# Performance work log

Hardware: AMD Instinct MI355X
Metric: run time of the kernel (lower is better)

## Reference

```python
import jax, jax.numpy as jnp
import numpy as np

S = 1024      # sequence length
V = 32000     # vocab size
H = 1024      # hidden_dim
A = 128       # attn_size (module default)


def lstm_cell(x, h, c, Wih, Whh, b):
    # torch LSTM gate order: i, f, g, o
    g = x @ Wih.T + h @ Whh.T + b
    i, f, gg, o = jnp.split(g, 4)
    c = jax.nn.sigmoid(f) * c + jax.nn.sigmoid(i) * jnp.tanh(gg)
    h = jax.nn.sigmoid(o) * jnp.tanh(c)
    return h, c


def setup_inputs() -> dict:
    key = jax.random.key(0)
    ks = jax.random.split(key, 16)
    p = lambda k, shape: (jax.random.normal(k, shape, jnp.float32) * 0.02)
    return {
        'input_seq': jax.random.randint(ks[0], (S,), 0, V),
        'gold_seq': jax.random.randint(ks[1], (S,), 0, V),
        'embed': p(ks[2], (V, H)),
        'enc_Wih': p(ks[3], (4 * H, H)),
        'enc_Whh': p(ks[4], (4 * H, H)),
        'enc_b': jnp.zeros((4 * H,), jnp.float32),   # b_ih + b_hh combined
        'dec_Wih': p(ks[5], (4 * H, 2 * H)),          # decoder input = [prev, context]
        'dec_Whh': p(ks[6], (4 * H, H)),
        'dec_b': jnp.zeros((4 * H,), jnp.float32),
        'U_w': p(ks[7], (A, H)), 'U_b': jnp.zeros((A,), jnp.float32),
        'Wa_w': p(ks[8], (A, H)), 'Wa_b': jnp.zeros((A,), jnp.float32),
        'Va_w': p(ks[9], (1, A)), 'Va_b': jnp.zeros((1,), jnp.float32),
        'out_w': p(ks[10], (V, H)), 'out_b': jnp.zeros((V,), jnp.float32),
    }


def reference(input_seq, gold_seq, embed, enc_Wih, enc_Whh, enc_b,
              dec_Wih, dec_Whh, dec_b, U_w, U_b, Wa_w, Wa_b, Va_w, Va_b,
              out_w, out_b):
    Hd = embed.shape[1]
    x_emb = embed[input_seq]  # (S, H)

    def enc_step(carry, x):
        h, c = carry
        h, c = lstm_cell(x, h, c, enc_Wih, enc_Whh, enc_b)
        return (h, c), h

    zero = jnp.zeros((Hd,), x_emb.dtype)
    (h0, c0), enc_out = jax.lax.scan(enc_step, (zero, zero), x_emb)  # enc_out: (S, H)

    U_enc = enc_out @ U_w.T + U_b  # (S, A), hidden-independent part of additive attention

    # teacher forcing: prev_0 = zeros, prev_i = embed(gold[i-1]); relu applied each step
    prev = jnp.concatenate([jnp.zeros((1, Hd), x_emb.dtype), embed[gold_seq[:-1]]], axis=0)
    prev = jax.nn.relu(prev)  # (S, H)

    def dec_step(carry, p):
        h, c = carry
        # additive attention scores: V(tanh(U(enc) + W(h)))  -> (S, 1)
        scores = jnp.tanh(U_enc + h @ Wa_w.T + Wa_b) @ Va_w.T + Va_b
        # faithful to nn.Softmax() on a (S,1) tensor: torch picks dim=1 -> all ones
        w = jax.nn.softmax(scores, axis=1)  # (S, 1), == ones
        context = w[:, 0] @ enc_out         # (H,) == sum of encoder outputs
        x = jnp.concatenate([p, context])   # (2H,)
        h, c = lstm_cell(x, h, c, dec_Wih, dec_Whh, dec_b)
        logits = h @ out_w.T + out_b        # (V,)
        return (h, c), (logits, jnp.argmax(logits))

    _, (preds, idxs) = jax.lax.scan(dec_step, (h0, c0), prev)
    return preds, idxs  # (S, V) float logits, (S,) predicted ids
```

## Files before the change

### kernel.cpp

```cpp
#include <hip/hip_runtime.h>
#include <math.h>


#define S_LEN 1024
#define HDIM  1024
#define VDIM  32000

typedef float f4 __attribute__((ext_vector_type(4)));

__device__ __forceinline__ void agent_storef(float* p, float v) {
    __hip_atomic_store(p, v, __ATOMIC_RELAXED, __HIP_MEMORY_SCOPE_AGENT);
}
__device__ __forceinline__ float sigmoidf_(float x) {
    return 1.0f / (1.0f + expf(-x));
}
__device__ __forceinline__ void llc_load_4x4(const float* p, f4& a, f4& b,
                                             f4& c, f4& d) {
    asm volatile(
        "global_load_dwordx4 %0, %4, off sc0 sc1\n\t"
        "global_load_dwordx4 %1, %4, off offset:1024 sc0 sc1\n\t"
        "global_load_dwordx4 %2, %4, off offset:2048 sc0 sc1\n\t"
        "global_load_dwordx4 %3, %4, off offset:3072 sc0 sc1\n\t"
        "s_waitcnt vmcnt(0)"
        : "=&v"(a), "=&v"(b), "=&v"(c), "=&v"(d)
        : "v"(p) : "memory");
}
__device__ __forceinline__ int swz(int s) {
    return (s & ~7) | ((s ^ (s >> 3)) & 7);
}

template<int MODE>
__global__ __launch_bounds__(256)
void gemm_nt(const float* __restrict__ A, int lda,
             const float* __restrict__ B, int ldb,
             const float* __restrict__ bias,
             float* __restrict__ C, int ldc,
             const float* __restrict__ embed,
             const int* __restrict__ gidx,
             int M, int N, int K)
{
    __shared__ float As[16][128];
    __shared__ float Bs[16][128];

    const int tid = threadIdx.x;
    const int m0 = blockIdx.y * 128;
    const int n0 = blockIdx.x * 128;

    float acc[8][8];
#pragma unroll
    for (int r = 0; r < 8; ++r)
#pragma unroll
        for (int c = 0; c < 8; ++c) acc[r][c] = 0.0f;

    const int ty = tid >> 4;
    const int tx = tid & 15;

    for (int k0 = 0; k0 < K; k0 += 16) {
#pragma unroll
        for (int q = 0; q < 2; ++q) {
            int id = tid * 2 + q;
            int m  = id >> 2;
            int c4 = (id & 3) * 4;
            float4 v;
            if (MODE == 0) {
                v = *(const float4*)(A + (size_t)(m0 + m) * lda + k0 + c4);
            } else if (MODE == 1) {
                int row = gidx[m0 + m];
                v = *(const float4*)(embed + (size_t)row * HDIM + k0 + c4);
            } else {
                int mg = m0 + m;
                if (mg == 0) {
                    v = make_float4(0.f, 0.f, 0.f, 0.f);
                } else {
                    int row = gidx[mg - 1];
                    v = *(const float4*)(embed + (size_t)row * HDIM + k0 + c4);
                    v.x = fmaxf(v.x, 0.f); v.y = fmaxf(v.y, 0.f);
                    v.z = fmaxf(v.z, 0.f); v.w = fmaxf(v.w, 0.f);
                }
            }
            As[c4 + 0][m] = v.x; As[c4 + 1][m] = v.y;
            As[c4 + 2][m] = v.z; As[c4 + 3][m] = v.w;
        }
#pragma unroll
        for (int q = 0; q < 2; ++q) {
            int id = tid * 2 + q;
            int n  = id >> 2;
            int c4 = (id & 3) * 4;
            float4 v = *(const float4*)(B + (size_t)(n0 + n) * ldb + k0 + c4);
            Bs[c4 + 0][n] = v.x; Bs[c4 + 1][n] = v.y;
            Bs[c4 + 2][n] = v.z; Bs[c4 + 3][n] = v.w;
        }
        __syncthreads();

#pragma unroll
        for (int k = 0; k < 16; ++k) {
            float4 a0 = *(const float4*)&As[k][ty * 8];
            float4 a1 = *(const float4*)&As[k][ty * 8 + 4];
            float4 b0 = *(const float4*)&Bs[k][tx * 8];
            float4 b1 = *(const float4*)&Bs[k][tx * 8 + 4];
            float av[8] = {a0.x,a0.y,a0.z,a0.w,a1.x,a1.y,a1.z,a1.w};
            float bv[8] = {b0.x,b0.y,b0.z,b0.w,b1.x,b1.y,b1.z,b1.w};
#pragma unroll
            for (int r = 0; r < 8; ++r)
#pragma unroll
                for (int c = 0; c < 8; ++c)
                    acc[r][c] = fmaf(av[r], bv[c], acc[r][c]);
        }
        __syncthreads();
    }

    const int mbase = m0 + ty * 8;
    const int nbase = n0 + tx * 8;
#pragma unroll
    for (int r = 0; r < 8; ++r) {
        float4 o0, o1;
        o0.x = acc[r][0] + bias[nbase + 0];
        o0.y = acc[r][1] + bias[nbase + 1];
        o0.z = acc[r][2] + bias[nbase + 2];
        o0.w = acc[r][3] + bias[nbase + 3];
        o1.x = acc[r][4] + bias[nbase + 4];
        o1.y = acc[r][5] + bias[nbase + 5];
        o1.z = acc[r][6] + bias[nbase + 6];
        o1.w = acc[r][7] + bias[nbase + 7];
        *(float4*)(C + (size_t)(mbase + r) * ldc + nbase)     = o0;
        *(float4*)(C + (size_t)(mbase + r) * ldc + nbase + 4) = o1;
    }
}

__global__ __launch_bounds__(512, 2)
void lstm_seq(const float* __restrict__ Whh,
              const float* __restrict__ G,
              const float* __restrict__ h_init,
              const float* __restrict__ c_init,
              float* __restrict__ h_out,
              float* __restrict__ c_fin,
              float* __restrict__ csum_out,
              int slen)
{
    __shared__ f4 hbuf[256];
    const int tid = threadIdx.x;
    const int g   = blockIdx.x;
    const int wv  = tid >> 6;
    const int lg  = tid & 63;
    const int j   = g * 8 + wv;

    f4 W[4][4];
#pragma unroll
    for (int q = 0; q < 4; ++q)
#pragma unroll
        for (int i = 0; i < 4; ++i)
            W[q][i] = *(const f4*)(Whh + (size_t)(j + q * HDIM) * HDIM
                                   + 4 * lg + 256 * i);

    float c = 0.0f, csum = 0.0f;
    if (lg == 0) c = c_init[j];

    float gnow = G[(size_t)(lg & 3) * HDIM + j];

    for (int t = 0; t < slen; ++t) {
#pragma unroll
        for (int q = 0; q < 4; ++q)
#pragma unroll
            for (int i = 0; i < 4; ++i)
                asm volatile("" : "+v"(W[q][i]));

        const float* hp = (t == 0) ? h_init : (h_out + (size_t)(t - 1) * HDIM);

        if (wv == 0) {
            f4 a, b, cc, d;
            const float* p = hp + 4 * lg;
            for (;;) {
                llc_load_4x4(p, a, b, cc, d);
                float s0 = (a.x + a.y) + (a.z + a.w);
                float s1 = (b.x + b.y) + (b.z + b.w);
                float s2 = (cc.x + cc.y) + (cc.z + cc.w);
                float s3 = (d.x + d.y) + (d.z + d.w);
                float s  = (s0 + s1) + (s2 + s3);
                if (!__any(s != s)) break;
                __builtin_amdgcn_s_sleep(1);
            }
            hbuf[swz(lg)]       = a;
            hbuf[swz(64 + lg)]  = b;
            hbuf[swz(128 + lg)] = cc;
            hbuf[swz(192 + lg)] = d;
        }
        __syncthreads();

        int tn = (t + 1 < slen) ? (t + 1) : t;
        float gnext = G[(size_t)tn * (4 * HDIM) + (lg & 3) * HDIM + j];

        f4 h0 = hbuf[swz(lg)];
        f4 h1 = hbuf[swz(64 + lg)];
        f4 h2 = hbuf[swz(128 + lg)];
        f4 h3 = hbuf[swz(192 + lg)];
        float p0 = 0.f, p1 = 0.f, p2 = 0.f, p3 = 0.f;
        f4 hv;
#pragma unroll
        for (int i = 0; i < 4; ++i) {
            hv = (i == 0) ? h0 : (i == 1) ? h1 : (i == 2) ? h2 : h3;
            p0 = fmaf(W[0][i].x, hv.x, fmaf(W[0][i].y, hv.y,
                 fmaf(W[0][i].z, hv.z, fmaf(W[0][i].w, hv.w, p0))));
            p1 = fmaf(W[1][i].x, hv.x, fmaf(W[1][i].y, hv.y,
                 fmaf(W[1][i].z, hv.z, fmaf(W[1][i].w, hv.w, p1))));
            p2 = fmaf(W[2][i].x, hv.x, fmaf(W[2][i].y, hv.y,
                 fmaf(W[2][i].z, hv.z, fmaf(W[2][i].w, hv.w, p2))));
            p3 = fmaf(W[3][i].x, hv.x, fmaf(W[3][i].y, hv.y,
                 fmaf(W[3][i].z, hv.z, fmaf(W[3][i].w, hv.w, p3))));
        }

        float t01 = __shfl_xor((lg & 1) ? p0 : p1, 1);
        float s01 = ((lg & 1) ? p1 : p0) + t01;
        float t23 = __shfl_xor((lg & 1) ? p2 : p3, 1);
        float s23 = ((lg & 1) ? p3 : p2) + t23;
        float tq  = __shfl_xor((lg & 2) ? s01 : s23, 2);
        float s   = ((lg & 2) ? s23 : s01) + tq;
        s += __shfl_xor(s, 4);
        s += __shfl_xor(s, 8);
        s += __shfl_xor(s, 16);
        s += __shfl_xor(s, 32);

        float pre = s + gnow;
        float act = ((lg & 3) == 2) ? tanhf(pre) : sigmoidf_(pre);
        float a1 = __shfl(act, 1);
        float a2 = __shfl(act, 2);
        float a3 = __shfl(act, 3);

        if (lg == 0) {
            c = a1 * c + act * a2;
            float h = a3 * tanhf(c);
            csum += h;
            agent_storef(h_out + (size_t)t * HDIM + j, h);
        }
        gnow = gnext;

        __syncthreads();
    }

    if (lg == 0) {
        if (c_fin)    c_fin[j]    = c;
        if (csum_out) csum_out[j] = csum;
    }
}

__global__ __launch_bounds__(256)
void ctx_bias_k(const float* __restrict__ dec_Wih,
                const float* __restrict__ dec_b,
                const float* __restrict__ ctx,
                float* __restrict__ out)
{
    const int wv = threadIdx.x >> 6;
    const int lane = threadIdx.x & 63;
    const int r = blockIdx.x * 4 + wv;
    const float* wr = dec_Wih + (size_t)r * (2 * HDIM) + HDIM;
    float s = 0.f;
    for (int k = lane; k < HDIM; k += 64) s += wr[k] * ctx[k];
#pragma unroll
    for (int off = 32; off > 0; off >>= 1) s += __shfl_xor(s, off);
    if (lane == 0) out[r] = s + dec_b[r];
}

__global__ __launch_bounds__(256)
void argmax_k(const float* __restrict__ logits, float* __restrict__ out_idx)
{
    __shared__ float bv[256];
    __shared__ int   bidx[256];
    const int row = blockIdx.x;
    const int tid = threadIdx.x;
    const float* p = logits + (size_t)row * VDIM;
    float best = -INFINITY;
    int   bi   = 0;
    for (int v = tid; v < VDIM; v += 256) {
        float x = p[v];
        if (x > best) { best = x; bi = v; }
    }
    bv[tid] = best; bidx[tid] = bi;
    __syncthreads();
    for (int s = 128; s > 0; s >>= 1) {
        if (tid < s) {
            if (bv[tid + s] > bv[tid] ||
                (bv[tid + s] == bv[tid] && bidx[tid + s] < bidx[tid])) {
                bv[tid] = bv[tid + s];
                bidx[tid] = bidx[tid + s];
            }
        }
        __syncthreads();
    }
    if (tid == 0) out_idx[row] = (float)bidx[0];
}

extern "C" void kernel_launch(void* const* d_in, const int* in_sizes, int n_in,
                              void* d_out, int out_size, void* d_ws, size_t ws_size,
                              hipStream_t stream)
{
    (void)in_sizes; (void)n_in; (void)out_size; (void)ws_size;

    const int*   input_seq = (const int*)d_in[0];
    const int*   gold_seq  = (const int*)d_in[1];
    const float* embed     = (const float*)d_in[2];
    const float* enc_Wih   = (const float*)d_in[3];
    const float* enc_Whh   = (const float*)d_in[4];
    const float* enc_b     = (const float*)d_in[5];
    const float* dec_Wih   = (const float*)d_in[6];
    const float* dec_Whh   = (const float*)d_in[7];
    const float* dec_b     = (const float*)d_in[8];
    const float* out_w     = (const float*)d_in[15];
    const float* out_b     = (const float*)d_in[16];

    float* out = (float*)d_out;

    float* G_enc = out;
    float* G_dec = out + 4194304;

    float* zerovec   = (float*)d_ws + 256;
    float* c0        = zerovec + 1024;
    float* ctx       = c0 + 1024;
    float* ctxb      = ctx + 1024;
    float* enc_out   = ctxb + 4096;
    float* dec_h     = enc_out + 1048576;

    hipMemsetAsync(d_ws, 0, 5120, stream);
    hipMemsetAsync(enc_out, 0xFF, (size_t)S_LEN * HDIM * 4, stream);
    hipMemsetAsync(dec_h,   0xFF, (size_t)S_LEN * HDIM * 4, stream);

    dim3 blk(256);

    gemm_nt<1><<<dim3(32, 8), blk, 0, stream>>>(
        nullptr, 0, enc_Wih, HDIM, enc_b, G_enc, 4 * HDIM,
        embed, input_seq, S_LEN, 4 * HDIM, HDIM);

    lstm_seq<<<128, dim3(512), 0, stream>>>(
        enc_Whh, G_enc, zerovec, zerovec, enc_out, c0, ctx, S_LEN);

    ctx_bias_k<<<1024, blk, 0, stream>>>(dec_Wih, dec_b, ctx, ctxb);

    gemm_nt<2><<<dim3(32, 8), blk, 0, stream>>>(
        nullptr, 0, dec_Wih, 2 * HDIM, ctxb, G_dec, 4 * HDIM,
        embed, gold_seq, S_LEN, 4 * HDIM, HDIM);

    lstm_seq<<<128, dim3(512), 0, stream>>>(
        dec_Whh, G_dec, enc_out + (size_t)(S_LEN - 1) * HDIM, c0,
        dec_h, nullptr, nullptr, S_LEN);

    gemm_nt<0><<<dim3(VDIM / 128, 8), blk, 0, stream>>>(
        dec_h, HDIM, out_w, HDIM, out_b, out, VDIM,
        nullptr, nullptr, S_LEN, VDIM, HDIM);

    argmax_k<<<1024, blk, 0, stream>>>(out, out + (size_t)S_LEN * VDIM);
}
```

Baseline: 5.335 ms.

## Use split-bf16 MFMA for logits GEMM with fused argmax and merged input GEMMs

Replaces the fp32 SIMT logits GEMM with a bf16 MFMA kernel that splits each fp32 operand into hi/lo bf16 parts and runs three MFMAs to keep near-fp32 accuracy. Argmax is fused into the GEMM epilogue through a packed 64-bit atomicMax key, which removes the separate pass that re-read the full logits matrix. The encoder and decoder input-projection GEMMs are merged into one launch, with the context bias added inside the decoder LSTM instead of inside the GEMM. The risks are numerical differences from the bf16 split possibly changing argmax ties, plus atomic contention.

```diff
diff --git a/kernel.cpp b/kernel.cpp
--- a/kernel.cpp
+++ b/kernel.cpp
@@ -7,6 +7,8 @@
 #define VDIM  32000
 
 typedef float f4 __attribute__((ext_vector_type(4)));
+typedef float f32x4 __attribute__((ext_vector_type(4)));
+typedef short short8 __attribute__((ext_vector_type(8)));
 
 __device__ __forceinline__ void agent_storef(float* p, float v) {
     __hip_atomic_store(p, v, __ATOMIC_RELAXED, __HIP_MEMORY_SCOPE_AGENT);
@@ -25,26 +27,39 @@
         : "=&v"(a), "=&v"(b), "=&v"(c), "=&v"(d)
         : "v"(p) : "memory");
 }
+__device__ __forceinline__ bool any_nan16(f4 a, f4 b, f4 c, f4 d) {
+    float s0 = (a.x + a.y) + (a.z + a.w);
+    float s1 = (b.x + b.y) + (b.z + b.w);
+    float s2 = (c.x + c.y) + (c.z + c.w);
+    float s3 = (d.x + d.y) + (d.z + d.w);
+    float s  = (s0 + s1) + (s2 + s3);
+    return s != s;
+}
 __device__ __forceinline__ int swz(int s) {
     return (s & ~7) | ((s ^ (s >> 3)) & 7);
 }
+__device__ __forceinline__ void split_bf16(float x, unsigned short& h,
+                                           unsigned short& l) {
+    unsigned u = __float_as_uint(x);
+    unsigned hr = (u + 0x7FFFu + ((u >> 16) & 1u)) >> 16;
+    h = (unsigned short)hr;
+    float hf = __uint_as_float(hr << 16);
+    float r = x - hf;
+    unsigned v = __float_as_uint(r);
+    l = (unsigned short)((v + 0x7FFFu + ((v >> 16) & 1u)) >> 16);
+}
 
 template<int MODE>
-__global__ __launch_bounds__(256)
-void gemm_nt(const float* __restrict__ A, int lda,
-             const float* __restrict__ B, int ldb,
-             const float* __restrict__ bias,
-             float* __restrict__ C, int ldc,
-             const float* __restrict__ embed,
-             const int* __restrict__ gidx,
-             int M, int N, int K)
+__device__ void gemm_body(const float* __restrict__ B, int ldb,
+                          const float* __restrict__ bias,
+                          float* __restrict__ C, int ldc,
+                          const float* __restrict__ embed,
+                          const int* __restrict__ gidx,
+                          int m0, int n0, int K)
 {
     __shared__ float As[16][128];
     __shared__ float Bs[16][128];
-
     const int tid = threadIdx.x;
-    const int m0 = blockIdx.y * 128;
-    const int n0 = blockIdx.x * 128;
 
     float acc[8][8];
 #pragma unroll
@@ -62,9 +77,7 @@
             int m  = id >> 2;
             int c4 = (id & 3) * 4;
             float4 v;
-            if (MODE == 0) {
-                v = *(const float4*)(A + (size_t)(m0 + m) * lda + k0 + c4);
-            } else if (MODE == 1) {
+            if (MODE == 1) {
                 int row = gidx[m0 + m];
                 v = *(const float4*)(embed + (size_t)row * HDIM + k0 + c4);
             } else {
@@ -91,7 +104,6 @@
             Bs[c4 + 2][n] = v.z; Bs[c4 + 3][n] = v.w;
         }
         __syncthreads();
-
 #pragma unroll
         for (int k = 0; k < 16; ++k) {
             float4 a0 = *(const float4*)&As[k][ty * 8];
@@ -114,28 +126,52 @@
 #pragma unroll
     for (int r = 0; r < 8; ++r) {
         float4 o0, o1;
-        o0.x = acc[r][0] + bias[nbase + 0];
-        o0.y = acc[r][1] + bias[nbase + 1];
-        o0.z = acc[r][2] + bias[nbase + 2];
-        o0.w = acc[r][3] + bias[nbase + 3];
-        o1.x = acc[r][4] + bias[nbase + 4];
-        o1.y = acc[r][5] + bias[nbase + 5];
-        o1.z = acc[r][6] + bias[nbase + 6];
-        o1.w = acc[r][7] + bias[nbase + 7];
+        float b0 = (MODE == 2) ? 0.f : bias[nbase + 0];
+        float b1 = (MODE == 2) ? 0.f : bias[nbase + 1];
+        float b2 = (MODE == 2) ? 0.f : bias[nbase + 2];
+        float b3 = (MODE == 2) ? 0.f : bias[nbase + 3];
+        float b4 = (MODE == 2) ? 0.f : bias[nbase + 4];
+        float b5 = (MODE == 2) ? 0.f : bias[nbase + 5];
+        float b6 = (MODE == 2) ? 0.f : bias[nbase + 6];
+        float b7 = (MODE == 2) ? 0.f : bias[nbase + 7];
+        o0.x = acc[r][0] + b0; o0.y = acc[r][1] + b1;
+        o0.z = acc[r][2] + b2; o0.w = acc[r][3] + b3;
+        o1.x = acc[r][4] + b4; o1.y = acc[r][5] + b5;
+        o1.z = acc[r][6] + b6; o1.w = acc[r][7] + b7;
         *(float4*)(C + (size_t)(mbase + r) * ldc + nbase)     = o0;
         *(float4*)(C + (size_t)(mbase + r) * ldc + nbase + 4) = o1;
     }
 }
 
-__global__ __launch_bounds__(512, 2)
-void lstm_seq(const float* __restrict__ Whh,
-              const float* __restrict__ G,
-              const float* __restrict__ h_init,
-              const float* __restrict__ c_init,
-              float* __restrict__ h_out,
-              float* __restrict__ c_fin,
-              float* __restrict__ csum_out,
-              int slen)
+__global__ __launch_bounds__(256)
+void g_both(const float* __restrict__ embed,
+            const int* __restrict__ input_seq,
+            const int* __restrict__ gold_seq,
+            const float* __restrict__ enc_Wih,
+            const float* __restrict__ enc_b,
+            const float* __restrict__ dec_Wih,
+            float* __restrict__ G_enc,
+            float* __restrict__ G_dec)
+{
+    const int bx = blockIdx.x, by = blockIdx.y;
+    if (by < 8)
+        gemm_body<1>(enc_Wih, HDIM, enc_b, G_enc, 4 * HDIM,
+                     embed, input_seq, by * 128, bx * 128, HDIM);
+    else
+        gemm_body<2>(dec_Wih, 2 * HDIM, nullptr, G_dec, 4 * HDIM,
+                     embed, gold_seq, (by - 8) * 128, bx * 128, HDIM);
+}
+
+template<int GCTX>
+__device__ void lstm_body(const float* __restrict__ Whh,
+                          const float* __restrict__ G,
+                          const float* __restrict__ gctx_vec,
+                          const float* __restrict__ h_init,
+                          const float* __restrict__ c_init,
+                          float* __restrict__ h_out,
+                          float* __restrict__ c_fin,
+                          float* __restrict__ csum_out,
+                          int slen)
 {
     __shared__ f4 hbuf[256];
     const int tid = threadIdx.x;
@@ -155,7 +191,10 @@
     float c = 0.0f, csum = 0.0f;
     if (lg == 0) c = c_init[j];
 
-    float gnow = G[(size_t)(lg & 3) * HDIM + j];
+    float gctx = 0.0f;
+    if (GCTX) gctx = gctx_vec[(size_t)(lg & 3) * HDIM + j];
+
+    float gnow = G[(size_t)(lg & 3) * HDIM + j] + gctx;
 
     for (int t = 0; t < slen; ++t) {
 #pragma unroll
@@ -171,12 +210,7 @@
             const float* p = hp + 4 * lg;
             for (;;) {
                 llc_load_4x4(p, a, b, cc, d);
-                float s0 = (a.x + a.y) + (a.z + a.w);
-                float s1 = (b.x + b.y) + (b.z + b.w);
-                float s2 = (cc.x + cc.y) + (cc.z + cc.w);
-                float s3 = (d.x + d.y) + (d.z + d.w);
-                float s  = (s0 + s1) + (s2 + s3);
-                if (!__any(s != s)) break;
+                if (!__any(any_nan16(a, b, cc, d))) break;
                 __builtin_amdgcn_s_sleep(1);
             }
             hbuf[swz(lg)]       = a;
@@ -187,7 +221,7 @@
         __syncthreads();
 
         int tn = (t + 1 < slen) ? (t + 1) : t;
-        float gnext = G[(size_t)tn * (4 * HDIM) + (lg & 3) * HDIM + j];
+        float gnext = G[(size_t)tn * (4 * HDIM) + (lg & 3) * HDIM + j] + gctx;
 
         f4 h0 = hbuf[swz(lg)];
         f4 h1 = hbuf[swz(64 + lg)];
@@ -232,7 +266,6 @@
             agent_storef(h_out + (size_t)t * HDIM + j, h);
         }
         gnow = gnext;
-
         __syncthreads();
     }
 
@@ -240,6 +273,24 @@
         if (c_fin)    c_fin[j]    = c;
         if (csum_out) csum_out[j] = csum;
     }
+}
+
+__global__ __launch_bounds__(512, 2)
+void lstm_seq(const float* __restrict__ Whh, const float* __restrict__ G,
+              const float* __restrict__ h_init, const float* __restrict__ c_init,
+              float* __restrict__ h_out, float* __restrict__ c_fin,
+              float* __restrict__ csum_out, int slen)
+{
+    lstm_body<0>(Whh, G, nullptr, h_init, c_init, h_out, c_fin, csum_out, slen);
+}
+
+__global__ __launch_bounds__(512, 2)
+void dec_lstm(const float* __restrict__ Whh, const float* __restrict__ G,
+              const float* __restrict__ ctxb, const float* __restrict__ h_init,
+              const float* __restrict__ c_init, float* __restrict__ h_out,
+              int slen)
+{
+    lstm_body<1>(Whh, G, ctxb, h_init, c_init, h_out, nullptr, nullptr, slen);
 }
 
 __global__ __launch_bounds__(256)
@@ -259,33 +310,121 @@
     if (lane == 0) out[r] = s + dec_b[r];
 }
 
+#define LSTR 40
+
+__global__ __launch_bounds__(256, 1)
+void logits_mfma(const float* __restrict__ Amat,
+                 const float* __restrict__ Bmat,
+                 const float* __restrict__ bias,
+                 float* __restrict__ C,
+                 unsigned long long* __restrict__ amax)
+{
+    __shared__ unsigned short Ah[128][LSTR], Al[128][LSTR];
+    __shared__ unsigned short Bh[128][LSTR], Bl[128][LSTR];
+
+    const int tid = threadIdx.x;
+    const int l   = tid & 63;
+    const int w   = tid >> 6;
+    const int n0  = blockIdx.x * 128;
+    const int m0  = blockIdx.y * 128;
+    const int mb  = (w >> 1) * 64;
+    const int nb  = (w & 1) * 64;
+
+    f32x4 acc[4][4];
+#pragma unroll
+    for (int i = 0; i < 4; ++i)
+#pragma unroll
+        for (int j = 0; j < 4; ++j) acc[i][j] = (f32x4){0.f, 0.f, 0.f, 0.f};
+
+    for (int k0 = 0; k0 < HDIM; k0 += 32) {
+#pragma unroll
+        for (int q = 0; q < 4; ++q) {
+            int id  = q * 256 + tid;
+            int row = id >> 3;
+            int kq  = (id & 7) * 4;
+            float4 av = *(const float4*)(Amat + (size_t)(m0 + row) * HDIM
+                                         + k0 + kq);
+            float4 bv = *(const float4*)(Bmat + (size_t)(n0 + row) * HDIM
+                                         + k0 + kq);
+            unsigned short h0,h1,h2,h3, l0,l1,l2,l3;
+            split_bf16(av.x, h0, l0); split_bf16(av.y, h1, l1);
+            split_bf16(av.z, h2, l2); split_bf16(av.w, h3, l3);
+            Ah[row][kq+0]=h0; Ah[row][kq+1]=h1; Ah[row][kq+2]=h2; Ah[row][kq+3]=h3;
+            Al[row][kq+0]=l0; Al[row][kq+1]=l1; Al[row][kq+2]=l2; Al[row][kq+3]=l3;
+            split_bf16(bv.x, h0, l0); split_bf16(bv.y, h1, l1);
+            split_bf16(bv.z, h2, l2); split_bf16(bv.w, h3, l3);
+            Bh[row][kq+0]=h0; Bh[row][kq+1]=h1; Bh[row][kq+2]=h2; Bh[row][kq+3]=h3;
+            Bl[row][kq+0]=l0; Bl[row][kq+1]=l1; Bl[row][kq+2]=l2; Bl[row][kq+3]=l3;
+        }
+        __syncthreads();
+
+        const int kb = (l >> 4) * 8;
+        short8 a_hi[4], a_lo[4], b_hi[4], b_lo[4];
+#pragma unroll
+        for (int i = 0; i < 4; ++i) {
+            int ra = mb + i * 16 + (l & 15);
+            int rb = nb + i * 16 + (l & 15);
+            a_hi[i] = *(const short8*)&Ah[ra][kb];
+            a_lo[i] = *(const short8*)&Al[ra][kb];
+            b_hi[i] = *(const short8*)&Bh[rb][kb];
+            b_lo[i] = *(const short8*)&Bl[rb][kb];
+        }
+#pragma unroll
+        for (int i = 0; i < 4; ++i)
+#pragma unroll
+            for (int j = 0; j < 4; ++j) {
+                acc[i][j] = __builtin_amdgcn_mfma_f32_16x16x32_bf16(
+                    a_hi[i], b_hi[j], acc[i][j], 0, 0, 0);
+                acc[i][j] = __builtin_amdgcn_mfma_f32_16x16x32_bf16(
+                    a_hi[i], b_lo[j], acc[i][j], 0, 0, 0);
+                acc[i][j] = __builtin_amdgcn_mfma_f32_16x16x32_bf16(
+                    a_lo[i], b_hi[j], acc[i][j], 0, 0, 0);
+            }
+        __syncthreads();
+    }
+
+#pragma unroll
+    for (int i = 0; i < 4; ++i) {
+        const int mrow = m0 + mb + i * 16 + ((l >> 4) << 2);
+        unsigned long long key[4] = {0ull, 0ull, 0ull, 0ull};
+#pragma unroll
+        for (int j = 0; j < 4; ++j) {
+            int n = n0 + nb + j * 16 + (l & 15);
+            float bv = bias[n];
+            f32x4 o = acc[i][j];
+#pragma unroll
+            for (int r = 0; r < 4; ++r) {
+                float val = o[r] + bv;
+                C[(size_t)(mrow + r) * VDIM + n] = val;
+                unsigned um = __float_as_uint(val);
+                um = (um & 0x80000000u) ? ~um : (um | 0x80000000u);
+                unsigned long long k2 = ((unsigned long long)um << 32)
+                    | (unsigned long long)(0xFFFFFFFFu - (unsigned)n);
+                if (k2 > key[r]) key[r] = k2;
+            }
+        }
+#pragma unroll
+        for (int r = 0; r < 4; ++r) {
+#pragma unroll
+            for (int off = 1; off < 16; off <<= 1) {
+                unsigned long long other = __shfl_xor(key[r], off);
+                if (other > key[r]) key[r] = other;
+            }
+            if ((l & 15) == 0)
+                atomicMax(&amax[mrow + r], key[r]);
+        }
+    }
+}
+
 __global__ __launch_bounds__(256)
-void argmax_k(const float* __restrict__ logits, float* __restrict__ out_idx)
-{
-    __shared__ float bv[256];
-    __shared__ int   bidx[256];
-    const int row = blockIdx.x;
-    const int tid = threadIdx.x;
-    const float* p = logits + (size_t)row * VDIM;
-    float best = -INFINITY;
-    int   bi   = 0;
-    for (int v = tid; v < VDIM; v += 256) {
-        float x = p[v];
-        if (x > best) { best = x; bi = v; }
-    }
-    bv[tid] = best; bidx[tid] = bi;
-    __syncthreads();
-    for (int s = 128; s > 0; s >>= 1) {
-        if (tid < s) {
-            if (bv[tid + s] > bv[tid] ||
-                (bv[tid + s] == bv[tid] && bidx[tid + s] < bidx[tid])) {
-                bv[tid] = bv[tid + s];
-                bidx[tid] = bidx[tid + s];
-            }
-        }
-        __syncthreads();
-    }
-    if (tid == 0) out_idx[row] = (float)bidx[0];
+void idx_final(const unsigned long long* __restrict__ amax,
+               float* __restrict__ out_idx)
+{
+    int i = blockIdx.x * 256 + threadIdx.x;
+    if (i < S_LEN) {
+        unsigned col = 0xFFFFFFFFu - (unsigned)(amax[i] & 0xFFFFFFFFull);
+        out_idx[i] = (float)col;
+    }
 }
 
 extern "C" void kernel_launch(void* const* d_in, const int* in_sizes, int n_in,
@@ -307,43 +446,36 @@
     const float* out_b     = (const float*)d_in[16];
 
     float* out = (float*)d_out;
-
     float* G_enc = out;
     float* G_dec = out + 4194304;
 
-    float* zerovec   = (float*)d_ws + 256;
-    float* c0        = zerovec + 1024;
-    float* ctx       = c0 + 1024;
-    float* ctxb      = ctx + 1024;
-    float* enc_out   = ctxb + 4096;
-    float* dec_h     = enc_out + 1048576;
-
-    hipMemsetAsync(d_ws, 0, 5120, stream);
+    char* wsb = (char*)d_ws;
+    unsigned long long* amax = (unsigned long long*)wsb;
+    float* zerovec = (float*)(wsb + 8192);
+    float* c0      = zerovec + 1024;
+    float* ctx     = c0 + 1024;
+    float* ctxb    = ctx + 1024;
+    float* enc_out = ctxb + 4096;
+    float* dec_h   = enc_out + 1048576;
+
+    hipMemsetAsync(d_ws, 0, 12288, stream);
     hipMemsetAsync(enc_out, 0xFF, (size_t)S_LEN * HDIM * 4, stream);
     hipMemsetAsync(dec_h,   0xFF, (size_t)S_LEN * HDIM * 4, stream);
 
-    dim3 blk(256);
-
-    gemm_nt<1><<<dim3(32, 8), blk, 0, stream>>>(
-        nullptr, 0, enc_Wih, HDIM, enc_b, G_enc, 4 * HDIM,
-        embed, input_seq, S_LEN, 4 * HDIM, HDIM);
-
-    lstm_seq<<<128, dim3(512), 0, stream>>>(
+    g_both<<<dim3(32, 16), 256, 0, stream>>>(
+        embed, input_seq, gold_seq, enc_Wih, enc_b, dec_Wih, G_enc, G_dec);
+
+    lstm_seq<<<128, 512, 0, stream>>>(
         enc_Whh, G_enc, zerovec, zerovec, enc_out, c0, ctx, S_LEN);
 
-    ctx_bias_k<<<1024, blk, 0, stream>>>(dec_Wih, dec_b, ctx, ctxb);
-
-    gemm_nt<2><<<dim3(32, 8), blk, 0, stream>>>(
-        nullptr, 0, dec_Wih, 2 * HDIM, ctxb, G_dec, 4 * HDIM,
-        embed, gold_seq, S_LEN, 4 * HDIM, HDIM);
-
-    lstm_seq<<<128, dim3(512), 0, stream>>>(
-        dec_Whh, G_dec, enc_out + (size_t)(S_LEN - 1) * HDIM, c0,
-        dec_h, nullptr, nullptr, S_LEN);
-
-    gemm_nt<0><<<dim3(VDIM / 128, 8), blk, 0, stream>>>(
-        dec_h, HDIM, out_w, HDIM, out_b, out, VDIM,
-        nullptr, nullptr, S_LEN, VDIM, HDIM);
-
-    argmax_k<<<1024, blk, 0, stream>>>(out, out + (size_t)S_LEN * VDIM);
-}
+    ctx_bias_k<<<1024, 256, 0, stream>>>(dec_Wih, dec_b, ctx, ctxb);
+
+    dec_lstm<<<128, 512, 0, stream>>>(
+        dec_Whh, G_dec, ctxb, enc_out + (size_t)(S_LEN - 1) * HDIM, c0,
+        dec_h, S_LEN);
+
+    logits_mfma<<<dim3(VDIM / 128, S_LEN / 128), 256, 0, stream>>>(
+        dec_h, out_w, out_b, out, amax);
+
+    idx_final<<<4, 256, 0, stream>>>(amax, out + (size_t)S_LEN * VDIM);
+}
```

New measurement: 6.598 ms. 1.24x slower.
